# Performance work log

Measured on AMD Instinct MI355X. Metric: run time of the kernel, lower is better.

The kernel has to match this reference:

```python
import jax, jax.numpy as jnp
import numpy as np

B, C, H, W = 32, 3, 512, 512


def expm_affine(theta):
    # theta: [B, 2, 3] -> pad to 3x3 with a zero bottom row, matrix-exp, keep top 2 rows
    zero_row = jnp.zeros((theta.shape[0], 1, 3), theta.dtype)
    A = jnp.concatenate([theta, zero_row], axis=1)  # [B,3,3]
    E = jax.vmap(jax.scipy.linalg.expm)(A)
    return E[:, :2, :]


def affine_grid(theta23, h, w):
    # torch F.affine_grid with align_corners=False: pixel-center normalized coords
    xs = (2.0 * jnp.arange(w, dtype=theta23.dtype) + 1.0) / w - 1.0  # [W]
    ys = (2.0 * jnp.arange(h, dtype=theta23.dtype) + 1.0) / h - 1.0  # [H]
    gx, gy = jnp.meshgrid(xs, ys)  # [H,W] each
    base = jnp.stack([gx, gy, jnp.ones_like(gx)], axis=-1)  # [H,W,3]
    # grid[b,h,w,j] = sum_k theta[b,j,k] * base[h,w,k]; j=0 -> x, j=1 -> y
    return jnp.einsum('hwk,bjk->bhwj', base, theta23)  # [B,H,W,2]


def grid_sample(img, grid):
    # bilinear, zeros padding, align_corners=False (torch defaults)
    b, c, h, w = img.shape
    ix = (grid[..., 0] + 1.0) * (w * 0.5) - 0.5  # [B,Ho,Wo]
    iy = (grid[..., 1] + 1.0) * (h * 0.5) - 0.5
    x0 = jnp.floor(ix)
    y0 = jnp.floor(iy)
    x1, y1 = x0 + 1.0, y0 + 1.0
    wa = (x1 - ix) * (y1 - iy)
    wb = (x1 - ix) * (iy - y0)
    wc = (ix - x0) * (y1 - iy)
    wd = (ix - x0) * (iy - y0)

    def fetch(xf, yf):
        valid = (xf >= 0) & (xf <= w - 1) & (yf >= 0) & (yf <= h - 1)
        xc = jnp.clip(xf, 0, w - 1).astype(jnp.int32)
        yc = jnp.clip(yf, 0, h - 1).astype(jnp.int32)
        v = jax.vmap(lambda im, y, x: im[:, y, x])(img, yc, xc)  # [B,C,Ho,Wo]
        return v * valid[:, None].astype(img.dtype)

    out = (fetch(x0, y0) * wa[:, None]
           + fetch(x0, y1) * wb[:, None]
           + fetch(x1, y0) * wc[:, None]
           + fetch(x1, y1) * wd[:, None])
    return out


def setup_inputs() -> dict:
    key = jax.random.key(0)
    kx, kt = jax.random.split(key)
    x = jax.random.normal(kx, (B, C, H, W), dtype=jnp.float32)
    theta = jax.random.normal(kt, (B, 6), dtype=jnp.float32)
    return {"x": x, "theta": theta}


def reference(x, theta):
    th = theta.reshape(-1, 2, 3)
    A = expm_affine(th)            # [B,2,3]
    grid = affine_grid(A, H, W)    # [B,H,W,2]
    return grid_sample(x, grid)    # [B,C,H,W]
```

## Files before the change

### kernel.cpp

```cpp
#include <hip/hip_runtime.h>
#include <math.h>

#define BB 32
#define CC 3
#define HH 512
#define WW 512

struct f2 { float a, b; };
__device__ __forceinline__ f2 load_f2(const float* __restrict__ p) {
    f2 r;
    __builtin_memcpy(&r, p, sizeof(f2));
    return r;
}

__global__ void expm_kernel(const float* __restrict__ theta, float* __restrict__ E) {
    int b = threadIdx.x;
    if (b >= BB) return;

    double A[3][3];
#pragma unroll
    for (int j = 0; j < 2; ++j)
#pragma unroll
        for (int k = 0; k < 3; ++k)
            A[j][k] = (double)theta[b * 6 + j * 3 + k];
    A[2][0] = A[2][1] = A[2][2] = 0.0;

    double nrm = 0.0;
#pragma unroll
    for (int i = 0; i < 3; ++i) {
        double r = fabs(A[i][0]) + fabs(A[i][1]) + fabs(A[i][2]);
        nrm = fmax(nrm, r);
    }
    int s = 0;
    while (nrm > 0.5) { nrm *= 0.5; ++s; }
    double sc = ldexp(1.0, -s);
#pragma unroll
    for (int i = 0; i < 3; ++i)
#pragma unroll
        for (int k = 0; k < 3; ++k) A[i][k] *= sc;

    double R[3][3] = {{1, 0, 0}, {0, 1, 0}, {0, 0, 1}};
    double T[3][3] = {{1, 0, 0}, {0, 1, 0}, {0, 0, 1}};
#pragma unroll
    for (int k = 1; k <= 14; ++k) {
        double N[3][3];
        const double inv = 1.0 / (double)k;
#pragma unroll
        for (int i = 0; i < 3; ++i)
#pragma unroll
            for (int j = 0; j < 3; ++j)
                N[i][j] = (T[i][0] * A[0][j] + T[i][1] * A[1][j] + T[i][2] * A[2][j]) * inv;
#pragma unroll
        for (int i = 0; i < 3; ++i)
#pragma unroll
            for (int j = 0; j < 3; ++j) {
                T[i][j] = N[i][j];
                R[i][j] += N[i][j];
            }
    }
    for (int q = 0; q < s; ++q) {
        double N[3][3];
#pragma unroll
        for (int i = 0; i < 3; ++i)
#pragma unroll
            for (int j = 0; j < 3; ++j)
                N[i][j] = R[i][0] * R[0][j] + R[i][1] * R[1][j] + R[i][2] * R[2][j];
#pragma unroll
        for (int i = 0; i < 3; ++i)
#pragma unroll
            for (int j = 0; j < 3; ++j) R[i][j] = N[i][j];
    }

#pragma unroll
    for (int j = 0; j < 2; ++j)
#pragma unroll
        for (int k = 0; k < 3; ++k)
            E[b * 6 + j * 3 + k] = (float)R[j][k];
}

__global__ __launch_bounds__(256) void st_sample_kernel(const float* __restrict__ x,
                                                        const float* __restrict__ E,
                                                        float* __restrict__ out) {
    const int bid = blockIdx.x;
    const int b = bid >> 10;
    const int t = bid & 1023;
    const int tileY = t >> 5, tileX = t & 31;

    const int tid = threadIdx.x;
    const int wv = tid >> 6, lane = tid & 63;
    const int px = (tileX << 4) + ((wv & 1) << 3) + (lane & 7);
    const int py = (tileY << 4) + ((wv >> 1) << 3) + (lane >> 3);

    const float t00 = E[b * 6 + 0], t01 = E[b * 6 + 1], t02 = E[b * 6 + 2];
    const float t10 = E[b * 6 + 3], t11 = E[b * 6 + 4], t12 = E[b * 6 + 5];

    const float* __restrict__ xb = x + (size_t)b * CC * HH * WW;

    const float gx = (2.0f * (float)px + 1.0f) * (1.0f / (float)WW) - 1.0f;
    const float gy = (2.0f * (float)py + 1.0f) * (1.0f / (float)HH) - 1.0f;
    const float grid_x = t00 * gx + t01 * gy + t02;
    const float grid_y = t10 * gx + t11 * gy + t12;
    const float ix = (grid_x + 1.0f) * ((float)WW * 0.5f) - 0.5f;
    const float iy = (grid_y + 1.0f) * ((float)HH * 0.5f) - 0.5f;

    float acc[CC] = {0.0f, 0.0f, 0.0f};

    const bool any = (ix > -1.0f) & (ix < (float)WW) & (iy > -1.0f) & (iy < (float)HH);
    if (any) {
        float x0f = floorf(ix), y0f = floorf(iy);
        float x1f = x0f + 1.0f, y1f = y0f + 1.0f;
        float wa = (x1f - ix) * (y1f - iy);
        float wb = (x1f - ix) * (iy - y0f);
        float wc = (ix - x0f) * (y1f - iy);
        float wd = (ix - x0f) * (iy - y0f);

        float mx0 = (x0f >= 0.0f) ? 1.0f : 0.0f;
        float mx1 = (x1f <= (float)(WW - 1)) ? 1.0f : 0.0f;
        float my0 = (y0f >= 0.0f) ? 1.0f : 0.0f;
        float my1 = (y1f <= (float)(HH - 1)) ? 1.0f : 0.0f;

        int xi0 = (int)fminf(fmaxf(x0f, 0.0f), (float)(WW - 1));
        int xi1 = (int)fminf(fmaxf(x1f, 0.0f), (float)(WW - 1));
        int yi0 = (int)fminf(fmaxf(y0f, 0.0f), (float)(HH - 1));
        int yi1 = (int)fminf(fmaxf(y1f, 0.0f), (float)(HH - 1));

        int bx = min(xi0, WW - 2);
        int d0 = xi0 - bx;
        int d1 = xi1 - bx;
        int ib0 = yi0 * WW + bx;
        int ib1 = yi1 * WW + bx;

        float wA = wa * mx0 * my0;
        float wB = wb * mx0 * my1;
        float wC = wc * mx1 * my0;
        float wD = wd * mx1 * my1;

        f2 r0[CC], r1[CC];
#pragma unroll
        for (int c = 0; c < CC; ++c) {
            const float* __restrict__ xc = xb + c * (HH * WW);
            r0[c] = load_f2(xc + ib0);
            r1[c] = load_f2(xc + ib1);
        }
#pragma unroll
        for (int c = 0; c < CC; ++c) {
            float v00 = d0 ? r0[c].b : r0[c].a;
            float v10 = d1 ? r0[c].b : r0[c].a;
            float v01 = d0 ? r1[c].b : r1[c].a;
            float v11 = d1 ? r1[c].b : r1[c].a;
            acc[c] = wA * v00 + wB * v01 + wC * v10 + wD * v11;
        }
    }

    const size_t obase = ((size_t)b * CC) * (HH * WW) + (size_t)py * WW + px;
#pragma unroll
    for (int c = 0; c < CC; ++c)
        out[obase + (size_t)c * (HH * WW)] = acc[c];
}

extern "C" void kernel_launch(void* const* d_in, const int* in_sizes, int n_in,
                              void* d_out, int out_size, void* d_ws, size_t ws_size,
                              hipStream_t stream) {
    const float* x = (const float*)d_in[0];
    const float* theta = (const float*)d_in[1];
    float* out = (float*)d_out;
    float* E = (float*)d_ws;

    expm_kernel<<<1, 64, 0, stream>>>(theta, E);

    const int nblocks = BB * 32 * 32;
    st_sample_kernel<<<nblocks, 256, 0, stream>>>(x, E, out);
}
```

Baseline: 209.8 us.

## Stage per-tile source footprint in LDS for bilinear gathers

Computes each output tile's source bounding box from its four corner coordinates. When the box fits in 64x64 and is non-empty, the block cooperatively loads all three channels into shared memory, and the bilinear taps then read from LDS. Other tiles fall back to the previous global f2 gather path. This aims to replace scattered global reads with coalesced ones, at the cost of 48KB of LDS per block, a barrier, and extra redundant loads.

```diff
diff --git a/kernel.cpp b/kernel.cpp
--- a/kernel.cpp
+++ b/kernel.cpp
@@ -81,27 +81,60 @@
 __global__ __launch_bounds__(256) void st_sample_kernel(const float* __restrict__ x,
                                                         const float* __restrict__ E,
                                                         float* __restrict__ out) {
+    __shared__ float lds[CC * 64 * 64];
+
     const int bid = blockIdx.x;
     const int b = bid >> 10;
     const int t = bid & 1023;
     const int tileY = t >> 5, tileX = t & 31;
+    const int tx0 = tileX << 4, ty0 = tileY << 4;
 
     const int tid = threadIdx.x;
     const int wv = tid >> 6, lane = tid & 63;
-    const int px = (tileX << 4) + ((wv & 1) << 3) + (lane & 7);
-    const int py = (tileY << 4) + ((wv >> 1) << 3) + (lane >> 3);
+    const int px = tx0 + ((wv & 1) << 3) + (lane & 7);
+    const int py = ty0 + ((wv >> 1) << 3) + (lane >> 3);
 
     const float t00 = E[b * 6 + 0], t01 = E[b * 6 + 1], t02 = E[b * 6 + 2];
     const float t10 = E[b * 6 + 3], t11 = E[b * 6 + 4], t12 = E[b * 6 + 5];
 
     const float* __restrict__ xb = x + (size_t)b * CC * HH * WW;
 
+    const float cgx0 = (2.0f * (float)tx0 + 1.0f) * (1.0f / (float)WW) - 1.0f;
+    const float cgx1 = (2.0f * (float)(tx0 + 15) + 1.0f) * (1.0f / (float)WW) - 1.0f;
+    const float cgy0 = (2.0f * (float)ty0 + 1.0f) * (1.0f / (float)HH) - 1.0f;
+    const float cgy1 = (2.0f * (float)(ty0 + 15) + 1.0f) * (1.0f / (float)HH) - 1.0f;
+    #define CIX(gx, gy) (((t00 * (gx) + t01 * (gy) + t02) + 1.0f) * ((float)WW * 0.5f) - 0.5f)
+    #define CIY(gx, gy) (((t10 * (gx) + t11 * (gy) + t12) + 1.0f) * ((float)HH * 0.5f) - 0.5f)
+    const float ix00 = CIX(cgx0, cgy0), ix10 = CIX(cgx1, cgy0), ix01 = CIX(cgx0, cgy1), ix11 = CIX(cgx1, cgy1);
+    const float iy00 = CIY(cgx0, cgy0), iy10 = CIY(cgx1, cgy0), iy01 = CIY(cgx0, cgy1), iy11 = CIY(cgx1, cgy1);
+    const float min_ix = fminf(fminf(ix00, ix10), fminf(ix01, ix11));
+    const float max_ix = fmaxf(fmaxf(ix00, ix10), fmaxf(ix01, ix11));
+    const float min_iy = fminf(fminf(iy00, iy10), fminf(iy01, iy11));
+    const float max_iy = fmaxf(fmaxf(iy00, iy10), fmaxf(iy01, iy11));
+    const int fb_x0 = (int)floorf(min_ix), fb_x1 = (int)floorf(max_ix) + 1;
+    const int fb_y0 = (int)floorf(min_iy), fb_y1 = (int)floorf(max_iy) + 1;
+    const bool empty = (fb_x1 < 0) | (fb_x0 > WW - 1) | (fb_y1 < 0) | (fb_y0 > HH - 1);
+    const int bb_x0 = max(fb_x0, 0), bb_x1 = min(fb_x1, WW - 1);
+    const int bb_y0 = max(fb_y0, 0), bb_y1 = min(fb_y1, HH - 1);
+    const int bw = bb_x1 - bb_x0 + 1, bh = bb_y1 - bb_y0 + 1;
+    const bool use_lds = (!empty) & (bw <= 64) & (bh <= 64);
+
+    if (use_lds) {
+#pragma unroll
+        for (int c = 0; c < CC; ++c) {
+            const float* __restrict__ xc = xb + c * (HH * WW) + (size_t)bb_y0 * WW + bb_x0;
+            float* __restrict__ lc = lds + c * 4096;
+            for (int r = wv; r < bh; r += 4) {
+                if (lane < bw) lc[(r << 6) + lane] = xc[r * WW + lane];
+            }
+        }
+        __syncthreads();
+    }
+
     const float gx = (2.0f * (float)px + 1.0f) * (1.0f / (float)WW) - 1.0f;
     const float gy = (2.0f * (float)py + 1.0f) * (1.0f / (float)HH) - 1.0f;
-    const float grid_x = t00 * gx + t01 * gy + t02;
-    const float grid_y = t10 * gx + t11 * gy + t12;
-    const float ix = (grid_x + 1.0f) * ((float)WW * 0.5f) - 0.5f;
-    const float iy = (grid_y + 1.0f) * ((float)HH * 0.5f) - 0.5f;
+    const float ix = CIX(gx, gy);
+    const float iy = CIY(gx, gy);
 
     float acc[CC] = {0.0f, 0.0f, 0.0f};
 
@@ -124,31 +157,42 @@
         int yi0 = (int)fminf(fmaxf(y0f, 0.0f), (float)(HH - 1));
         int yi1 = (int)fminf(fmaxf(y1f, 0.0f), (float)(HH - 1));
 
-        int bx = min(xi0, WW - 2);
-        int d0 = xi0 - bx;
-        int d1 = xi1 - bx;
-        int ib0 = yi0 * WW + bx;
-        int ib1 = yi1 * WW + bx;
-
         float wA = wa * mx0 * my0;
         float wB = wb * mx0 * my1;
         float wC = wc * mx1 * my0;
         float wD = wd * mx1 * my1;
 
-        f2 r0[CC], r1[CC];
-#pragma unroll
-        for (int c = 0; c < CC; ++c) {
-            const float* __restrict__ xc = xb + c * (HH * WW);
-            r0[c] = load_f2(xc + ib0);
-            r1[c] = load_f2(xc + ib1);
-        }
-#pragma unroll
-        for (int c = 0; c < CC; ++c) {
-            float v00 = d0 ? r0[c].b : r0[c].a;
-            float v10 = d1 ? r0[c].b : r0[c].a;
-            float v01 = d0 ? r1[c].b : r1[c].a;
-            float v11 = d1 ? r1[c].b : r1[c].a;
-            acc[c] = wA * v00 + wB * v01 + wC * v10 + wD * v11;
+        if (use_lds) {
+            const int lx0 = xi0 - bb_x0, lx1 = xi1 - bb_x0;
+            const int r0 = (yi0 - bb_y0) << 6, r1 = (yi1 - bb_y0) << 6;
+#pragma unroll
+            for (int c = 0; c < CC; ++c) {
+                const float* __restrict__ lc = lds + c * 4096;
+                float v00 = lc[r0 + lx0];
+                float v10 = lc[r0 + lx1];
+                float v01 = lc[r1 + lx0];
+                float v11 = lc[r1 + lx1];
+                acc[c] = wA * v00 + wB * v01 + wC * v10 + wD * v11;
+            }
+        } else {
+            int bx = min(xi0, WW - 2);
+            int d0 = xi0 - bx, d1 = xi1 - bx;
+            int ib0 = yi0 * WW + bx, ib1 = yi1 * WW + bx;
+            f2 r0[CC], r1[CC];
+#pragma unroll
+            for (int c = 0; c < CC; ++c) {
+                const float* __restrict__ xc = xb + c * (HH * WW);
+                r0[c] = load_f2(xc + ib0);
+                r1[c] = load_f2(xc + ib1);
+            }
+#pragma unroll
+            for (int c = 0; c < CC; ++c) {
+                float v00 = d0 ? r0[c].b : r0[c].a;
+                float v10 = d1 ? r0[c].b : r0[c].a;
+                float v01 = d0 ? r1[c].b : r1[c].a;
+                float v11 = d1 ? r1[c].b : r1[c].a;
+                acc[c] = wA * v00 + wB * v01 + wC * v10 + wD * v11;
+            }
         }
     }
 
```

Result: slower. 341.0 us (+62.5%).
